# Kernel tuning notes

Measured on AMD Instinct MI355X. Metric: run time of the kernel, lower is better.

## Reference

```python
import jax, jax.numpy as jnp
import numpy as np

NC = 32          # number of cells
NDIM = 1         # 1D CPAB
NSTEPS = 32      # nstepsolver


def _expm_affine1d(A):
    """Closed-form matrix exponential of [[a, b], [0, 0]] (batched).

    A: [M, 1, 2] -> returns [M, 2, 2] with expm = [[e^a, b*phi(a)], [0, 1]],
    phi(a) = (e^a - 1)/a, with a stable small-a branch.
    """
    a = A[:, 0, 0]
    b = A[:, 0, 1]
    small = jnp.abs(a) < 1e-6
    a_safe = jnp.where(small, 1.0, a)
    phi = jnp.where(small, 1.0 + 0.5 * a, jnp.expm1(a_safe) / a_safe)
    top = jnp.stack([jnp.exp(a), b * phi], axis=-1)            # [M, 2]
    bot = jnp.broadcast_to(jnp.array([0.0, 1.0], dtype=A.dtype), top.shape)
    return jnp.stack([top, bot], axis=-2)                       # [M, 2, 2]


def setup_inputs() -> dict:
    key = jax.random.key(0)
    k1, k2, k3 = jax.random.split(key, 3)
    n_points, n_theta, d = 262144, 8, 30
    points = jax.random.uniform(k1, (NDIM, n_points), dtype=jnp.float32)
    theta = 0.5 * jax.random.normal(k2, (n_theta, d), dtype=jnp.float32)
    basis = 0.3 * jax.random.normal(k3, ((NDIM + 1) * NDIM * NC, d), dtype=jnp.float32)
    return {"points": points, "theta": theta, "basis": basis}


def reference(points, theta, basis):
    n_points = points.shape[1]
    n_theta = theta.shape[0]
    dT = 1.0 / NSTEPS

    # Per-cell affine velocity matrices: Avees [2*nC, n_theta] -> As [n_theta*nC, 1, 2]
    Avees = basis @ theta.T
    As = Avees.T.reshape(n_theta * NC, NDIM, NDIM + 1)
    Trels = _expm_affine1d(dT * As)                               # [n_theta*nC, 2, 2]

    # Repeat points per theta (theta-major flatten order, matching torch code)
    x = jnp.tile(points[0], n_theta)                              # [N]
    pts = jnp.stack([x, jnp.ones_like(x)], axis=-1)               # [N, 2] homogeneous
    batch_idx = NC * jnp.repeat(jnp.arange(n_theta, dtype=jnp.int32), n_points)

    def step(p, _):
        cell = jnp.clip(jnp.floor(p[:, 0] * NC), 0, NC - 1).astype(jnp.int32)
        T = Trels[cell + batch_idx]                               # [N, 2, 2] gather
        return jnp.einsum('nij,nj->ni', T, p), None

    pts, _ = jax.lax.scan(step, pts, None, length=NSTEPS)

    # [N, 1] -> [n_theta, ndim, n_points]
    return pts[:, :NDIM].reshape(n_theta, n_points, NDIM).transpose(0, 2, 1)
```

## Files before the change

### kernel.cpp

```cpp
#include <hip/hip_runtime.h>
#include <math.h>

#define NC 32
#define NSTEPS 32

constexpr int BLOCK = 256;
constexpr int PTS_PER_THREAD = 4;
constexpr int CHUNK = BLOCK * PTS_PER_THREAD;

__global__ void trels_kernel(const float* __restrict__ theta,
                             const float* __restrict__ basis,
                             float2* __restrict__ trels,
                             int n_theta, int d) {
    int i = threadIdx.x;
    if (i >= n_theta * NC) return;
    int j = i / NC;
    int c = i % NC;
    float a = 0.0f, b = 0.0f;
    for (int k = 0; k < d; ++k) {
        float th = theta[j * d + k];
        a = fmaf(basis[(2 * c) * d + k],     th, a);
        b = fmaf(basis[(2 * c + 1) * d + k], th, b);
    }
    const float dT = 1.0f / (float)NSTEPS;
    a *= dT;
    b *= dT;
    float A = expf(a);
    float phi = (fabsf(a) < 1e-6f) ? (1.0f + 0.5f * a) : (expm1f(a) / a);
    trels[i] = make_float2(A, b * phi);
}

__global__ void __launch_bounds__(BLOCK)
step_kernel(const float* __restrict__ points,
            const float2* __restrict__ trels,
            float* __restrict__ out,
            int n_points) {
    __shared__ float2 tab[NC];
    int blocks_per_theta = n_points / CHUNK;
    int j = blockIdx.x / blocks_per_theta;
    int base = (blockIdx.x % blocks_per_theta) * CHUNK + threadIdx.x;

    if (threadIdx.x < NC) tab[threadIdx.x] = trels[j * NC + threadIdx.x];
    __syncthreads();

    float x[PTS_PER_THREAD];
#pragma unroll
    for (int i = 0; i < PTS_PER_THREAD; ++i)
        x[i] = points[base + i * BLOCK];

#pragma unroll
    for (int s = 0; s < NSTEPS; ++s) {
#pragma unroll
        for (int i = 0; i < PTS_PER_THREAD; ++i) {
            int c = (int)floorf(x[i] * (float)NC);
            c = c < 0 ? 0 : (c > NC - 1 ? NC - 1 : c);
            float2 t = tab[c];
            x[i] = fmaf(t.x, x[i], t.y);
        }
    }

#pragma unroll
    for (int i = 0; i < PTS_PER_THREAD; ++i)
        out[j * n_points + base + i * BLOCK] = x[i];
}

extern "C" void kernel_launch(void* const* d_in, const int* in_sizes, int n_in,
                              void* d_out, int out_size, void* d_ws, size_t ws_size,
                              hipStream_t stream) {
    const float* points = (const float*)d_in[0];
    const float* theta  = (const float*)d_in[1];
    const float* basis  = (const float*)d_in[2];

    int n_points = in_sizes[0];
    int d        = in_sizes[2] / (2 * NC);
    int n_theta  = in_sizes[1] / d;

    float2* trels = (float2*)d_ws;

    trels_kernel<<<1, 256, 0, stream>>>(theta, basis, trels, n_theta, d);

    int grid = n_theta * (n_points / CHUNK);
    step_kernel<<<grid, BLOCK, 0, stream>>>(points, trels, (float*)d_out, n_points);
}
```

Measured before the change: 74.42 us.

## Fuse Trels computation into step kernel and vectorize point I/O

Removes the separate single-block trels kernel, so each block computes its own 32-entry affine table in shared memory from theta and basis. This drops a kernel launch and the serialization between the two kernels. In exchange, every block redoes the small dot products and exp calls. Point loads and stores now use float4 per thread instead of strided scalars, and the cell clamp is done in float.

```diff
diff --git a/kernel.cpp b/kernel.cpp
--- a/kernel.cpp
+++ b/kernel.cpp
@@ -8,60 +8,57 @@
 constexpr int PTS_PER_THREAD = 4;
 constexpr int CHUNK = BLOCK * PTS_PER_THREAD;
 
-__global__ void trels_kernel(const float* __restrict__ theta,
-                             const float* __restrict__ basis,
-                             float2* __restrict__ trels,
-                             int n_theta, int d) {
-    int i = threadIdx.x;
-    if (i >= n_theta * NC) return;
-    int j = i / NC;
-    int c = i % NC;
-    float a = 0.0f, b = 0.0f;
-    for (int k = 0; k < d; ++k) {
-        float th = theta[j * d + k];
-        a = fmaf(basis[(2 * c) * d + k],     th, a);
-        b = fmaf(basis[(2 * c + 1) * d + k], th, b);
+__global__ void __launch_bounds__(BLOCK)
+cpab_kernel(const float* __restrict__ points,
+            const float* __restrict__ theta,
+            const float* __restrict__ basis,
+            float* __restrict__ out,
+            int n_points, int d) {
+    __shared__ float2 tab[NC];
+
+    const int blocks_per_theta = n_points / CHUNK;
+    const int j = blockIdx.x / blocks_per_theta;
+    const int tid = threadIdx.x;
+
+    if (tid < NC) {
+        const int c = tid;
+        const float* __restrict__ th = theta + j * d;
+        const float* __restrict__ ba = basis + (2 * c) * d;
+        const float* __restrict__ bb = basis + (2 * c + 1) * d;
+        float a = 0.0f, b = 0.0f;
+#pragma unroll 6
+        for (int k = 0; k < d; ++k) {
+            float t = th[k];
+            a = fmaf(ba[k], t, a);
+            b = fmaf(bb[k], t, b);
+        }
+        const float dT = 1.0f / (float)NSTEPS;
+        a *= dT;
+        b *= dT;
+        float A = expf(a);
+        float phi = (fabsf(a) < 1e-6f) ? (1.0f + 0.5f * a) : (expm1f(a) / a);
+        tab[c] = make_float2(A, b * phi);
     }
-    const float dT = 1.0f / (float)NSTEPS;
-    a *= dT;
-    b *= dT;
-    float A = expf(a);
-    float phi = (fabsf(a) < 1e-6f) ? (1.0f + 0.5f * a) : (expm1f(a) / a);
-    trels[i] = make_float2(A, b * phi);
-}
-
-__global__ void __launch_bounds__(BLOCK)
-step_kernel(const float* __restrict__ points,
-            const float2* __restrict__ trels,
-            float* __restrict__ out,
-            int n_points) {
-    __shared__ float2 tab[NC];
-    int blocks_per_theta = n_points / CHUNK;
-    int j = blockIdx.x / blocks_per_theta;
-    int base = (blockIdx.x % blocks_per_theta) * CHUNK + threadIdx.x;
-
-    if (threadIdx.x < NC) tab[threadIdx.x] = trels[j * NC + threadIdx.x];
     __syncthreads();
 
-    float x[PTS_PER_THREAD];
-#pragma unroll
-    for (int i = 0; i < PTS_PER_THREAD; ++i)
-        x[i] = points[base + i * BLOCK];
+    const int base = (blockIdx.x % blocks_per_theta) * CHUNK + tid * 4;
+
+    float4 v = *(const float4*)(points + base);
+    float x[PTS_PER_THREAD] = {v.x, v.y, v.z, v.w};
 
 #pragma unroll
     for (int s = 0; s < NSTEPS; ++s) {
 #pragma unroll
         for (int i = 0; i < PTS_PER_THREAD; ++i) {
-            int c = (int)floorf(x[i] * (float)NC);
-            c = c < 0 ? 0 : (c > NC - 1 ? NC - 1 : c);
-            float2 t = tab[c];
+            float cf = fminf(fmaxf(floorf(x[i] * (float)NC), 0.0f),
+                             (float)(NC - 1));
+            float2 t = tab[(int)cf];
             x[i] = fmaf(t.x, x[i], t.y);
         }
     }
 
-#pragma unroll
-    for (int i = 0; i < PTS_PER_THREAD; ++i)
-        out[j * n_points + base + i * BLOCK] = x[i];
+    float4 o = make_float4(x[0], x[1], x[2], x[3]);
+    *(float4*)(out + j * n_points + base) = o;
 }
 
 extern "C" void kernel_launch(void* const* d_in, const int* in_sizes, int n_in,
@@ -75,10 +72,7 @@
     int d        = in_sizes[2] / (2 * NC);
     int n_theta  = in_sizes[1] / d;
 
-    float2* trels = (float2*)d_ws;
-
-    trels_kernel<<<1, 256, 0, stream>>>(theta, basis, trels, n_theta, d);
-
     int grid = n_theta * (n_points / CHUNK);
-    step_kernel<<<grid, BLOCK, 0, stream>>>(points, trels, (float*)d_out, n_points);
+    cpab_kernel<<<grid, BLOCK, 0, stream>>>(points, theta, basis,
+                                            (float*)d_out, n_points, d);
 }
```

Result: no change. 74.09 us (-0.4%).

## Bin-sort points so each wavefront shares a cell and skips per-point lookups

Applied to the files above, without the earlier changes.

Adds a histogram, scan and scatter pass that bucket the points into 1024 bins by value, so each wavefront processes 512 nearby points. While the wavefront's min/max bounds stay in one cell, the main kernel applies a single uniform affine update instead of a per-point cell lookup from shared memory. Points are prescaled by 32 and loaded and stored with float4. An unpermute pass restores the original order. This adds several launches, atomics and a gather pass, in exchange for removing divergent LDS lookups and per-point cell computation in the 32-step loop.

```diff
diff --git a/kernel.cpp b/kernel.cpp
--- a/kernel.cpp
+++ b/kernel.cpp
@@ -3,65 +3,158 @@
 
 #define NC 32
 #define NSTEPS 32
-
-constexpr int BLOCK = 256;
-constexpr int PTS_PER_THREAD = 4;
-constexpr int CHUNK = BLOCK * PTS_PER_THREAD;
+#define NB 1024
 
 __global__ void trels_kernel(const float* __restrict__ theta,
                              const float* __restrict__ basis,
                              float2* __restrict__ trels,
                              int n_theta, int d) {
-    int i = threadIdx.x;
+    int i = blockIdx.x * blockDim.x + threadIdx.x;
     if (i >= n_theta * NC) return;
-    int j = i / NC;
-    int c = i % NC;
+    int j = i / NC, c = i % NC;
     float a = 0.0f, b = 0.0f;
     for (int k = 0; k < d; ++k) {
-        float th = theta[j * d + k];
-        a = fmaf(basis[(2 * c) * d + k],     th, a);
-        b = fmaf(basis[(2 * c + 1) * d + k], th, b);
+        float t = theta[j * d + k];
+        a = fmaf(basis[(2 * c) * d + k],     t, a);
+        b = fmaf(basis[(2 * c + 1) * d + k], t, b);
     }
     const float dT = 1.0f / (float)NSTEPS;
-    a *= dT;
-    b *= dT;
+    a *= dT; b *= dT;
     float A = expf(a);
     float phi = (fabsf(a) < 1e-6f) ? (1.0f + 0.5f * a) : (expm1f(a) / a);
-    trels[i] = make_float2(A, b * phi);
+    trels[i] = make_float2(A, 32.0f * (b * phi));
 }
 
-__global__ void __launch_bounds__(BLOCK)
-step_kernel(const float* __restrict__ points,
-            const float2* __restrict__ trels,
-            float* __restrict__ out,
-            int n_points) {
+__global__ void hist_kernel(const float* __restrict__ pts,
+                            unsigned* __restrict__ hist, int n) {
+    __shared__ unsigned lh[NB];
+    for (int b = threadIdx.x; b < NB; b += blockDim.x) lh[b] = 0;
+    __syncthreads();
+    for (int i = blockIdx.x * blockDim.x + threadIdx.x; i < n;
+         i += gridDim.x * blockDim.x) {
+        float x = pts[i];
+        int b = (int)(x * (float)NB);
+        b = b < 0 ? 0 : (b > NB - 1 ? NB - 1 : b);
+        atomicAdd(&lh[b], 1u);
+    }
+    __syncthreads();
+    for (int b = threadIdx.x; b < NB; b += blockDim.x)
+        if (lh[b]) atomicAdd(&hist[b], lh[b]);
+}
+
+__global__ void scan_kernel(unsigned* __restrict__ hist) {
+    __shared__ unsigned s0[NB], s1[NB];
+    int t = threadIdx.x;
+    unsigned v = hist[t];
+    s0[t] = v;
+    __syncthreads();
+    unsigned* src = s0; unsigned* dst = s1;
+    for (int off = 1; off < NB; off <<= 1) {
+        unsigned x = src[t];
+        if (t >= off) x += src[t - off];
+        dst[t] = x;
+        __syncthreads();
+        unsigned* tmp = src; src = dst; dst = tmp;
+    }
+    hist[t] = src[t] - v;
+}
+
+__global__ void scatter_kernel(const float* __restrict__ pts,
+                               unsigned* __restrict__ cursor,
+                               float* __restrict__ bx,
+                               unsigned* __restrict__ inv, int n) {
+    int i = blockIdx.x * blockDim.x + threadIdx.x;
+    if (i >= n) return;
+    float x = pts[i];
+    int b = (int)(x * (float)NB);
+    b = b < 0 ? 0 : (b > NB - 1 ? NB - 1 : b);
+    unsigned p = atomicAdd(&cursor[b], 1u);
+    bx[p] = x;
+    inv[i] = p;
+}
+
+__global__ void __launch_bounds__(256)
+main_kernel(const float* __restrict__ bx, const float2* __restrict__ trels,
+            float* __restrict__ obin, int n_points) {
     __shared__ float2 tab[NC];
-    int blocks_per_theta = n_points / CHUNK;
-    int j = blockIdx.x / blocks_per_theta;
-    int base = (blockIdx.x % blocks_per_theta) * CHUNK + threadIdx.x;
 
-    if (threadIdx.x < NC) tab[threadIdx.x] = trels[j * NC + threadIdx.x];
+    const int lane = threadIdx.x & 63;
+    const int wid  = threadIdx.x >> 6;
+    const int chunks = n_points >> 9;
+    const int gw = blockIdx.x * 4 + wid;
+    const int j = gw / chunks;
+    const int chunk = gw % chunks;
+    const int base = (chunk << 9) + lane * 8;
+
+    if (threadIdx.x < NC)
+        tab[threadIdx.x] = trels[j * NC + threadIdx.x];
     __syncthreads();
 
-    float x[PTS_PER_THREAD];
+    float y[8];
+    {
+        float4 v0 = *(const float4*)(bx + base);
+        float4 v1 = *(const float4*)(bx + base + 4);
+        y[0] = v0.x * 32.0f; y[1] = v0.y * 32.0f;
+        y[2] = v0.z * 32.0f; y[3] = v0.w * 32.0f;
+        y[4] = v1.x * 32.0f; y[5] = v1.y * 32.0f;
+        y[6] = v1.z * 32.0f; y[7] = v1.w * 32.0f;
+    }
+
+    float ylo = y[0], yhi = y[0];
 #pragma unroll
-    for (int i = 0; i < PTS_PER_THREAD; ++i)
-        x[i] = points[base + i * BLOCK];
+    for (int i = 1; i < 8; ++i) {
+        ylo = fminf(ylo, y[i]); yhi = fmaxf(yhi, y[i]);
+    }
+#pragma unroll
+    for (int off = 32; off; off >>= 1) {
+        ylo = fminf(ylo, __shfl_xor(ylo, off, 64));
+        yhi = fmaxf(yhi, __shfl_xor(yhi, off, 64));
+    }
 
+    for (int s = 0; s < NSTEPS; ++s) {
+        float cflo = fminf(fmaxf(floorf(ylo), 0.0f), 31.0f);
+        float cfhi = fminf(fmaxf(floorf(yhi), 0.0f), 31.0f);
+        if (cflo == cfhi) {
+            float2 t = tab[(int)cflo];
 #pragma unroll
-    for (int s = 0; s < NSTEPS; ++s) {
+            for (int i = 0; i < 8; ++i) y[i] = fmaf(t.x, y[i], t.y);
+            ylo = fmaf(t.x, ylo, t.y);
+            yhi = fmaf(t.x, yhi, t.y);
+        } else {
+            int clo = (int)cflo, chi = (int)cfhi;
 #pragma unroll
-        for (int i = 0; i < PTS_PER_THREAD; ++i) {
-            int c = (int)floorf(x[i] * (float)NC);
-            c = c < 0 ? 0 : (c > NC - 1 ? NC - 1 : c);
-            float2 t = tab[c];
-            x[i] = fmaf(t.x, x[i], t.y);
+            for (int i = 0; i < 8; ++i) {
+                float cf = fminf(fmaxf(floorf(y[i]), 0.0f), 31.0f);
+                float2 t = tab[(int)cf];
+                y[i] = fmaf(t.x, y[i], t.y);
+            }
+            float nlo = 3.0e38f, nhi = -3.0e38f;
+            for (int c = clo; c <= chi; ++c) {
+                float2 t = tab[c];
+                nlo = fminf(nlo, fmaf(t.x, ylo, t.y));
+                nhi = fmaxf(nhi, fmaf(t.x, yhi, t.y));
+            }
+            ylo = nlo; yhi = nhi;
         }
     }
 
-#pragma unroll
-    for (int i = 0; i < PTS_PER_THREAD; ++i)
-        out[j * n_points + base + i * BLOCK] = x[i];
+    const float inv32 = 1.0f / 32.0f;
+    float* op = obin + j * n_points + base;
+    float4 o0 = make_float4(y[0]*inv32, y[1]*inv32, y[2]*inv32, y[3]*inv32);
+    float4 o1 = make_float4(y[4]*inv32, y[5]*inv32, y[6]*inv32, y[7]*inv32);
+    *(float4*)op       = o0;
+    *(float4*)(op + 4) = o1;
+}
+
+__global__ void unperm_kernel(const float* __restrict__ obin,
+                              const unsigned* __restrict__ inv,
+                              float* __restrict__ out,
+                              int n_points, int n_theta) {
+    int i = blockIdx.x * blockDim.x + threadIdx.x;
+    if (i >= n_points) return;
+    unsigned p = inv[i];
+    for (int t = 0; t < n_theta; ++t)
+        out[t * n_points + i] = obin[t * n_points + p];
 }
 
 extern "C" void kernel_launch(void* const* d_in, const int* in_sizes, int n_in,
@@ -75,10 +168,24 @@
     int d        = in_sizes[2] / (2 * NC);
     int n_theta  = in_sizes[1] / d;
 
-    float2* trels = (float2*)d_ws;
+    char* ws = (char*)d_ws;
+    float*    bx    = (float*)ws;
+    unsigned* invp  = (unsigned*)(ws + (size_t)n_points * 4);
+    unsigned* hist  = (unsigned*)(ws + (size_t)n_points * 8);
+    float2*   trels = (float2*)(ws + (size_t)n_points * 8 + 8192);
+    float*    obin  = (float*)(ws + (size_t)n_points * 8 + 16384);
 
+    hipMemsetAsync(hist, 0, NB * sizeof(unsigned), stream);
     trels_kernel<<<1, 256, 0, stream>>>(theta, basis, trels, n_theta, d);
+    hist_kernel<<<256, 256, 0, stream>>>(points, hist, n_points);
+    scan_kernel<<<1, NB, 0, stream>>>(hist);
+    scatter_kernel<<<(n_points + 255) / 256, 256, 0, stream>>>(
+        points, hist, bx, invp, n_points);
 
-    int grid = n_theta * (n_points / CHUNK);
-    step_kernel<<<grid, BLOCK, 0, stream>>>(points, trels, (float*)d_out, n_points);
+    int chunks = n_points >> 9;
+    main_kernel<<<n_theta * chunks / 4, 256, 0, stream>>>(
+        bx, trels, obin, n_points);
+
+    unperm_kernel<<<(n_points + 255) / 256, 256, 0, stream>>>(
+        obin, invp, (float*)d_out, n_points, n_theta);
 }
```

New measurement: 209.9 us. 182% more time.

## Precompose 32-step piecewise-affine flow into a fine-bin lookup table with fallback

Applied to the files above, without the earlier changes.

Because every input point feeds the same 32-step per-theta piecewise-affine map, the change precomputes, for each of 8192 input bins, the composed affine map (scale and offset) and marks bins whose endpoints stay in the same cell sequence as pure. The main kernel then does a single table lookup and one FMA per point, replacing 32 dependent gather-FMA steps. Points in impure bins are appended to a global list via atomics and recomputed step by step in a fallback kernel. This adds three extra launches, a memset and atomic traffic, and the composed result may differ slightly in rounding from step-by-step evaluation.

```diff
diff --git a/kernel.cpp b/kernel.cpp
--- a/kernel.cpp
+++ b/kernel.cpp
@@ -3,65 +3,136 @@
 
 #define NC 32
 #define NSTEPS 32
-
-constexpr int BLOCK = 256;
-constexpr int PTS_PER_THREAD = 4;
-constexpr int CHUNK = BLOCK * PTS_PER_THREAD;
+#define NB 8192
 
 __global__ void trels_kernel(const float* __restrict__ theta,
                              const float* __restrict__ basis,
-                             float2* __restrict__ trels,
+                             float* __restrict__ tabs,
                              int n_theta, int d) {
     int i = threadIdx.x;
     if (i >= n_theta * NC) return;
-    int j = i / NC;
-    int c = i % NC;
+    int j = i >> 5, c = i & 31;
     float a = 0.0f, b = 0.0f;
     for (int k = 0; k < d; ++k) {
-        float th = theta[j * d + k];
-        a = fmaf(basis[(2 * c) * d + k],     th, a);
-        b = fmaf(basis[(2 * c + 1) * d + k], th, b);
+        float t = theta[j * d + k];
+        a = fmaf(basis[(2 * c) * d + k],     t, a);
+        b = fmaf(basis[(2 * c + 1) * d + k], t, b);
     }
     const float dT = 1.0f / (float)NSTEPS;
-    a *= dT;
-    b *= dT;
+    a *= dT; b *= dT;
     float A = expf(a);
     float phi = (fabsf(a) < 1e-6f) ? (1.0f + 0.5f * a) : (expm1f(a) / a);
-    trels[i] = make_float2(A, b * phi);
+    tabs[j * 64 + c]      = A;
+    tabs[j * 64 + 32 + c] = 32.0f * (b * phi);
 }
 
-__global__ void __launch_bounds__(BLOCK)
-step_kernel(const float* __restrict__ points,
-            const float2* __restrict__ trels,
-            float* __restrict__ out,
-            int n_points) {
-    __shared__ float2 tab[NC];
-    int blocks_per_theta = n_points / CHUNK;
-    int j = blockIdx.x / blocks_per_theta;
-    int base = (blockIdx.x % blocks_per_theta) * CHUNK + threadIdx.x;
-
-    if (threadIdx.x < NC) tab[threadIdx.x] = trels[j * NC + threadIdx.x];
+__global__ void __launch_bounds__(256)
+compose_kernel(const float* __restrict__ tabs,
+               float2* __restrict__ ST) {
+    __shared__ float tb[64];
+    const int j  = blockIdx.x >> 5;
+    const int i0 = (blockIdx.x & 31) * 256;
+    if (threadIdx.x < 64) tb[threadIdx.x] = tabs[j * 64 + threadIdx.x];
     __syncthreads();
 
-    float x[PTS_PER_THREAD];
+    const int i = i0 + threadIdx.x;
+    float zlo = (float)i * 0.00390625f;
+    float zhi = __uint_as_float(
+        __float_as_uint((float)(i + 1) * 0.00390625f) - 1u);
+    double Sd = 1.0, Td = 0.0;
+    bool pure = true;
 #pragma unroll
-    for (int i = 0; i < PTS_PER_THREAD; ++i)
-        x[i] = points[base + i * BLOCK];
+    for (int s = 0; s < NSTEPS; ++s) {
+        float flo = fminf(fmaxf(zlo, 0.0f), 31.5f);
+        float fhi = fminf(fmaxf(zhi, 0.0f), 31.5f);
+        int clo = (int)flo, chi = (int)fhi;
+        pure = pure && (clo == chi);
+        float Al = tb[clo],  Bl = tb[32 + clo];
+        float Ah = tb[chi],  Bh = tb[32 + chi];
+        Sd *= (double)Al;
+        Td = fma((double)Al, Td, (double)Bl);
+        zlo = fmaf(Al, zlo, Bl);
+        zhi = fmaf(Ah, zhi, Bh);
+    }
+    float S = (float)Sd;
+    ST[j * NB + i] = make_float2(pure ? S : -S, (float)(Td * (1.0 / 32.0)));
+}
+
+constexpr int MT   = 512;
+constexpr int MPTS = 8;
+constexpr int MCHUNK = MT * MPTS;
+
+__global__ void __launch_bounds__(MT)
+main_kernel(const float* __restrict__ points,
+            const float2* __restrict__ ST,
+            float* __restrict__ out,
+            unsigned* __restrict__ list,
+            unsigned* __restrict__ cnt,
+            int n_points) {
+    __shared__ float2 st[NB];
+    __shared__ unsigned short ll[MCHUNK];
+    __shared__ unsigned lcnt, gbase;
+
+    const int bpt = n_points / MCHUNK;
+    const int j = blockIdx.x / bpt;
+    const int cbase = (blockIdx.x % bpt) * MCHUNK;
+    const int tid = threadIdx.x;
+
+    {
+        const float4* src = (const float4*)(ST + j * NB);
+        float4* dst = (float4*)st;
+        for (int k = tid; k < NB / 2; k += MT) dst[k] = src[k];
+    }
+    if (tid == 0) lcnt = 0;
+    __syncthreads();
 
 #pragma unroll
-    for (int s = 0; s < NSTEPS; ++s) {
-#pragma unroll
-        for (int i = 0; i < PTS_PER_THREAD; ++i) {
-            int c = (int)floorf(x[i] * (float)NC);
-            c = c < 0 ? 0 : (c > NC - 1 ? NC - 1 : c);
-            float2 t = tab[c];
-            x[i] = fmaf(t.x, x[i], t.y);
+    for (int i = 0; i < MPTS; ++i) {
+        int p = cbase + i * MT + tid;
+        float x = points[p];
+        float f = fminf(fmaxf(x * 8192.0f, 0.0f), 8191.5f);
+        float2 t = st[(int)f];
+        if (t.x > 0.0f) {
+            out[j * n_points + p] = fmaf(t.x, x, t.y);
+        } else {
+            unsigned s = atomicAdd(&lcnt, 1u);
+            ll[s] = (unsigned short)(i * MT + tid);
         }
     }
+    __syncthreads();
+    if (tid == 0 && lcnt) gbase = atomicAdd(cnt, lcnt);
+    __syncthreads();
+    unsigned jn = (unsigned)(j * n_points + cbase);
+    for (unsigned k = tid; k < lcnt; k += MT)
+        list[gbase + k] = jn + ll[k];
+}
 
+__global__ void __launch_bounds__(256)
+fallback_kernel(const float* __restrict__ points,
+                const float* __restrict__ tabs,
+                float* __restrict__ out,
+                const unsigned* __restrict__ list,
+                const unsigned* __restrict__ cnt,
+                int n_points, int n_theta) {
+    __shared__ float tb[512];
+    for (int k = threadIdx.x; k < n_theta * 64; k += 256) tb[k] = tabs[k];
+    __syncthreads();
+    unsigned n = *cnt;
+    for (unsigned k = blockIdx.x * 256 + threadIdx.x; k < n;
+         k += gridDim.x * 256) {
+        unsigned gid = list[k];
+        unsigned j = gid / (unsigned)n_points;
+        unsigned p = gid - j * (unsigned)n_points;
+        float z = points[p] * 32.0f;
+        int base = j * 64;
 #pragma unroll
-    for (int i = 0; i < PTS_PER_THREAD; ++i)
-        out[j * n_points + base + i * BLOCK] = x[i];
+        for (int s = 0; s < NSTEPS; ++s) {
+            float zc = fminf(fmaxf(z, 0.0f), 31.5f);
+            int c = (int)zc;
+            z = fmaf(tb[base + c], z, tb[base + 32 + c]);
+        }
+        out[gid] = z * 0.03125f;
+    }
 }
 
 extern "C" void kernel_launch(void* const* d_in, const int* in_sizes, int n_in,
@@ -75,10 +146,17 @@
     int d        = in_sizes[2] / (2 * NC);
     int n_theta  = in_sizes[1] / d;
 
-    float2* trels = (float2*)d_ws;
+    char* ws = (char*)d_ws;
+    float*    tabs = (float*)ws;
+    float2*   ST   = (float2*)(ws + 4096);
+    unsigned* cnt  = (unsigned*)(ws + (1 << 20));
+    unsigned* list = (unsigned*)(ws + (1 << 20) + 4096);
 
-    trels_kernel<<<1, 256, 0, stream>>>(theta, basis, trels, n_theta, d);
-
-    int grid = n_theta * (n_points / CHUNK);
-    step_kernel<<<grid, BLOCK, 0, stream>>>(points, trels, (float*)d_out, n_points);
+    hipMemsetAsync(cnt, 0, sizeof(unsigned), stream);
+    trels_kernel<<<1, 256, 0, stream>>>(theta, basis, tabs, n_theta, d);
+    compose_kernel<<<n_theta * (NB / 256), 256, 0, stream>>>(tabs, ST);
+    main_kernel<<<n_theta * (n_points / MCHUNK), MT, 0, stream>>>(
+        points, ST, (float*)d_out, list, cnt, n_points);
+    fallback_kernel<<<512, 256, 0, stream>>>(
+        points, tabs, (float*)d_out, list, cnt, n_points, n_theta);
 }
```

New measurement: 90.19 us. 1.21x slower.
